# Optimization experiments

Hardware: AMD Instinct MI355X
Metric: run time of the kernel (lower is better)

The kernel has to match this reference:

```python
import jax, jax.numpy as jnp
import numpy as np

B, T, E, H, M = 1, 2048, 1536, 16, 3
KVH = 8
NREP = H // KVH
HD = E // H // M  # 32
EPS = 1e-5


def setup_inputs() -> dict:
    key = jax.random.key(0)
    ks = jax.random.split(key, 6)
    x = jax.random.normal(ks[0], (B, T, E), jnp.float32)
    # true rotary tables: freqs = pos * 10000^{-2i/d}, shape [T, HD//2]
    inv_freq = 1.0 / (10000.0 ** (np.arange(0, HD, 2, dtype=np.float64) / HD))
    ang = np.outer(np.arange(T, dtype=np.float64), inv_freq)
    cos = jnp.asarray(np.cos(ang), jnp.float32)
    sin = jnp.asarray(np.sin(ang), jnp.float32)
    s = 0.02
    q_w = s * jax.random.normal(ks[1], (M, E // M, E), jnp.float32)
    k_w = s * jax.random.normal(ks[2], (M, E // M // NREP, E), jnp.float32)
    v_w = s * jax.random.normal(ks[3], (E // NREP, E), jnp.float32)
    out_w = s * jax.random.normal(ks[4], (E, E), jnp.float32)
    raw_map_weights = jnp.array([0.1, -0.1, 0.1], jnp.float32)
    weight_scale = jnp.ones((1,), jnp.float32)
    subln_w = jnp.ones((M * HD,), jnp.float32)
    return dict(x=x, cos=cos, sin=sin, q_w=q_w, k_w=k_w, v_w=v_w,
                out_w=out_w, raw_map_weights=raw_map_weights,
                weight_scale=weight_scale, subln_w=subln_w)


def _rope_interleaved(t, cos, sin):
    # t: [..., seq, heads, hd]; cos/sin: [seq, hd//2]
    x1 = t[..., 0::2]
    x2 = t[..., 1::2]
    c = cos[:, None, :]
    s = sin[:, None, :]
    o1 = x1 * c - x2 * s
    o2 = x1 * s + x2 * c
    return jnp.stack([o1, o2], axis=-1).reshape(t.shape)


def reference(x, cos, sin, q_w, k_w, v_w, out_w, raw_map_weights, weight_scale, subln_w):
    b, t, e = x.shape
    m = q_w.shape[0]
    hd = 2 * cos.shape[-1]
    h = q_w.shape[1] // hd
    kvh = k_w.shape[1] // hd
    nrep = h // kvh
    scaling = hd ** -0.5

    map_w = jnp.tanh(raw_map_weights) * weight_scale  # [M]

    # per-map Q/K projections, all maps at once
    q = jnp.einsum('bte,mfe->mbtf', x, q_w).reshape(m, b, t, h, hd)
    k = jnp.einsum('bte,mfe->mbtf', x, k_w).reshape(m, b, t, kvh, hd)
    q = _rope_interleaved(q, cos, sin) * scaling
    k = _rope_interleaved(k, cos, sin)
    q = q.transpose(0, 1, 3, 2, 4)                      # [m,b,h,t,hd]
    k = jnp.repeat(k.transpose(0, 1, 3, 2, 4), nrep, axis=2)  # [m,b,h,t,hd]

    v = jnp.einsum('bte,fe->btf', x, v_w).reshape(b, t, kvh, m * hd)
    v = jnp.repeat(v.transpose(0, 2, 1, 3), nrep, axis=1)  # [b,h,t,m*hd]

    causal = jnp.where(jnp.triu(jnp.ones((t, t), bool), 1),
                       jnp.float32(-jnp.inf), jnp.float32(0.0))

    scores = jnp.einsum('mbhtd,mbhsd->mbhts', q, k)
    scores = jnp.nan_to_num(scores) + causal
    attn_w = jax.nn.softmax(scores.astype(jnp.float32), axis=-1).astype(x.dtype)
    combined = jnp.einsum('m,mbhts->bhts', map_w, attn_w)

    attn = jnp.einsum('bhts,bhsf->bhtf', combined, v)  # [b,h,t,m*hd]
    # RMSNorm over last dim
    var = jnp.mean(jnp.square(attn.astype(jnp.float32)), axis=-1, keepdims=True)
    attn = (attn * jax.lax.rsqrt(var + EPS)).astype(attn.dtype) * subln_w

    attn = attn.transpose(0, 2, 1, 3).reshape(b, t, h * m * hd)
    return jnp.einsum('bte,fe->btf', attn, out_w)
```

## Files before the change

kernel.cpp:

```cpp
#include <hip/hip_runtime.h>
#include <hip/hip_bf16.h>
#include <math.h>

#define T_DIM 2048
#define E_DIM 1536
#define K_DIM 1536

typedef unsigned short u16;
typedef unsigned int u32;
typedef __attribute__((ext_vector_type(8))) short bf16x8;
typedef __attribute__((ext_vector_type(4))) float f32x4;

__device__ __forceinline__ u16 f2bf(float x) {
    unsigned u = __float_as_uint(x);
    return (u16)((u + 0x7fffu + ((u >> 16) & 1u)) >> 16);
}

#define GLOAD16(gsrc, ldst)                                                              \
    __builtin_amdgcn_global_load_lds((const __attribute__((address_space(1))) u32*)(gsrc), \
                                     (__attribute__((address_space(3))) u32*)(ldst), 16, 0, 0)

__global__ __launch_bounds__(256) void cvt_bf16_5(const float* __restrict__ s0, u16* __restrict__ d0,
                                                  const float* __restrict__ s1, u16* __restrict__ d1,
                                                  const float* __restrict__ s2, u16* __restrict__ d2,
                                                  const float* __restrict__ s3, u16* __restrict__ d3,
                                                  const float* __restrict__ s4, u16* __restrict__ d4) {
    int i = blockIdx.x * 256 + threadIdx.x;
    const float* s;
    u16* d;
    int off;
    if (i < 786432)       { s = s0; d = d0; off = i; }
    else if (i < 1376256) { s = s1; d = d1; off = i - 786432; }
    else if (i < 1671168) { s = s2; d = d2; off = i - 1376256; }
    else if (i < 1966080) { s = s3; d = d3; off = i - 1671168; }
    else                  { s = s4; d = d4; off = i - 1966080; }
    float4 v = ((const float4*)s)[off];
    ((ushort4*)d)[off] = make_ushort4(f2bf(v.x), f2bf(v.y), f2bf(v.z), f2bf(v.w));
}

__global__ __launch_bounds__(256) void gemm_qkv_fused(const u16* __restrict__ A,
                                                      const u16* __restrict__ W,
                                                      const float* __restrict__ cosb,
                                                      const float* __restrict__ sinb,
                                                      u16* __restrict__ qb16,
                                                      u16* __restrict__ kpack,
                                                      u16* __restrict__ vpack,
                                                      float qscale) {
    const int K = K_DIM;
    __shared__ __align__(16) u16 As[128 * 64];
    __shared__ __align__(16) u16 Bs[128 * 64];
    const int tid = threadIdx.x;
    const int lane = tid & 63;
    const int wv = tid >> 6;
    const int wr = wv >> 1;
    const int wc = wv & 1;
    const int cl = lane & 15;
    const int g = lane >> 4;
    const int bm = blockIdx.y * 128;
    const int bn = blockIdx.x * 128;

    const char* Ab = (const char*)A;
    const char* Wb = (const char*)W;

    size_t a_src[4], b_src[4];
    int dst[4];
#pragma unroll
    for (int is = 0; is < 4; ++is) {
        int b = is * 4096 + tid * 16;
        int row = b >> 7;
        int wi = b & 127;
        dst[is] = b;
        a_src[is] = (size_t)(bm + row) * (K * 2) + (wi ^ ((row & 7) << 4));
        b_src[is] = (size_t)(bn + row) * (K * 2) + (wi ^ ((row & 7) << 4));
    }

    f32x4 acc[4][4];
#pragma unroll
    for (int mi = 0; mi < 4; ++mi)
#pragma unroll
        for (int ni = 0; ni < 4; ++ni) acc[mi][ni] = (f32x4){0.f, 0.f, 0.f, 0.f};

    for (int k0b = 0; k0b < K * 2; k0b += 128) {
#pragma unroll
        for (int is = 0; is < 4; ++is)
            GLOAD16(Ab + a_src[is] + k0b, (char*)As + dst[is]);
#pragma unroll
        for (int is = 0; is < 4; ++is)
            GLOAD16(Wb + b_src[is] + k0b, (char*)Bs + dst[is]);
        __syncthreads();
#pragma unroll
        for (int kk = 0; kk < 2; ++kk) {
            const int co = (kk * 64 + g * 16) ^ ((cl & 7) << 4);
            bf16x8 af[4], bfr[4];
#pragma unroll
            for (int mi = 0; mi < 4; ++mi)
                af[mi] = *(const bf16x8*)((const char*)As + (wr * 64 + mi * 16 + cl) * 128 + co);
#pragma unroll
            for (int ni = 0; ni < 4; ++ni)
                bfr[ni] = *(const bf16x8*)((const char*)Bs + (wc * 64 + ni * 16 + cl) * 128 + co);
#pragma unroll
            for (int mi = 0; mi < 4; ++mi)
#pragma unroll
                for (int ni = 0; ni < 4; ++ni)
                    acc[mi][ni] = __builtin_amdgcn_mfma_f32_16x16x32_bf16(af[mi], bfr[ni], acc[mi][ni], 0, 0, 0);
        }
        __syncthreads();
    }

    if (bn < 1536) {
#pragma unroll
        for (int mi = 0; mi < 4; ++mi)
#pragma unroll
            for (int ni = 0; ni < 4; ++ni)
#pragma unroll
                for (int r = 0; r < 4; ++r) {
                    int trow = bm + wr * 64 + mi * 16 + 4 * g + r;
                    int c = bn + wc * 64 + ni * 16 + cl;
                    float v = acc[mi][ni][r];
                    float pv = __shfl_xor(v, 1, 64);
                    int i = (c & 31) >> 1;
                    float cs = cosb[trow * 16 + i];
                    float sn = sinb[trow * 16 + i];
                    float o = v * cs + ((c & 1) ? pv * sn : -pv * sn);
                    qb16[(size_t)trow * E_DIM + c] = f2bf(o * qscale);
                }
    } else if (bn < 2304) {
#pragma unroll
        for (int mi = 0; mi < 4; ++mi)
#pragma unroll
            for (int ni = 0; ni < 4; ++ni)
#pragma unroll
                for (int r = 0; r < 4; ++r) {
                    int trow = bm + wr * 64 + mi * 16 + 4 * g + r;
                    int c = bn + wc * 64 + ni * 16 + cl;
                    float v = acc[mi][ni][r];
                    float pv = __shfl_xor(v, 1, 64);
                    int i = (c & 31) >> 1;
                    float cs = cosb[trow * 16 + i];
                    float sn = sinb[trow * 16 + i];
                    float o = v * cs + ((c & 1) ? pv * sn : -pv * sn);
                    int ck = c - 1536;
                    int m = ck >> 8;
                    int rem = ck & 255;
                    int kvhh = rem >> 5;
                    int d = rem & 31;
                    int cch = trow >> 5, st2 = (trow >> 4) & 1, colk = trow & 15;
                    size_t dstb = ((((size_t)(kvhh * 64 + cch) * 3 + m) * 2 + st2) * 16 + colk) * 32 + d;
                    kpack[dstb] = f2bf(o);
                }
    } else {
#pragma unroll
        for (int mi = 0; mi < 4; ++mi)
#pragma unroll
            for (int ni = 0; ni < 4; ++ni)
#pragma unroll
                for (int r = 0; r < 4; ++r) {
                    int trow = bm + wr * 64 + mi * 16 + 4 * g + r;
                    int c = bn + wc * 64 + ni * 16 + cl;
                    int fq = c - 2304;
                    int kvhh = fq / 96;
                    int f = fq - kvhh * 96;
                    size_t dstb = ((size_t)(kvhh * 64 + (trow >> 5)) * 96 + f) * 32 + (trow & 31);
                    vpack[dstb] = f2bf(acc[mi][ni][r]);
                }
    }
}

__global__ __launch_bounds__(256) void gemm_mfma_out(const u16* __restrict__ A,
                                                     const u16* __restrict__ W,
                                                     float* __restrict__ Cp,
                                                     int K, int ldC) {
    __shared__ __align__(16) u16 As[128 * 64];
    __shared__ __align__(16) u16 Bs[64 * 64];
    const int tid = threadIdx.x;
    const int lane = tid & 63;
    const int wv = tid >> 6;
    const int wr = wv >> 1;
    const int wc = wv & 1;
    const int cl = lane & 15;
    const int g = lane >> 4;
    const int bm = blockIdx.y * 128;
    const int bn = blockIdx.x * 64;

    const char* Ab = (const char*)A;
    const char* Wb = (const char*)W;

    size_t a_src[4];
    int a_dst[4];
#pragma unroll
    for (int is = 0; is < 4; ++is) {
        int b = is * 4096 + wv * 1024 + lane * 16;
        int row = b >> 7;
        int wi = b & 127;
        a_src[is] = (size_t)(bm + row) * (K * 2) + (wi ^ ((row & 7) << 4));
        a_dst[is] = b;
    }
    size_t b_src[2];
    int b_dst[2];
#pragma unroll
    for (int is = 0; is < 2; ++is) {
        int b = is * 4096 + wv * 1024 + lane * 16;
        int row = b >> 7;
        int wi = b & 127;
        b_src[is] = (size_t)(bn + row) * (K * 2) + (wi ^ ((row & 7) << 4));
        b_dst[is] = b;
    }

    f32x4 acc[4][2];
#pragma unroll
    for (int mi = 0; mi < 4; ++mi)
#pragma unroll
        for (int ni = 0; ni < 2; ++ni) acc[mi][ni] = (f32x4){0.f, 0.f, 0.f, 0.f};

    for (int k0b = 0; k0b < K * 2; k0b += 128) {
#pragma unroll
        for (int is = 0; is < 4; ++is)
            GLOAD16(Ab + a_src[is] + k0b, (char*)As + a_dst[is]);
#pragma unroll
        for (int is = 0; is < 2; ++is)
            GLOAD16(Wb + b_src[is] + k0b, (char*)Bs + b_dst[is]);
        __syncthreads();
#pragma unroll
        for (int kk = 0; kk < 2; ++kk) {
            const int co = (kk * 64 + g * 16) ^ ((cl & 7) << 4);
            bf16x8 af[4], bfr[2];
#pragma unroll
            for (int mi = 0; mi < 4; ++mi)
                af[mi] = *(const bf16x8*)((const char*)As + (wr * 64 + mi * 16 + cl) * 128 + co);
#pragma unroll
            for (int ni = 0; ni < 2; ++ni)
                bfr[ni] = *(const bf16x8*)((const char*)Bs + (wc * 32 + ni * 16 + cl) * 128 + co);
#pragma unroll
            for (int mi = 0; mi < 4; ++mi)
#pragma unroll
                for (int ni = 0; ni < 2; ++ni)
                    acc[mi][ni] = __builtin_amdgcn_mfma_f32_16x16x32_bf16(af[mi], bfr[ni], acc[mi][ni], 0, 0, 0);
        }
        __syncthreads();
    }

#pragma unroll
    for (int mi = 0; mi < 4; ++mi)
#pragma unroll
        for (int ni = 0; ni < 2; ++ni)
#pragma unroll
            for (int r = 0; r < 4; ++r) {
                size_t row = bm + wr * 64 + mi * 16 + 4 * g + r;
                size_t col = bn + wc * 32 + ni * 16 + cl;
                Cp[row * ldC + col] = acc[mi][ni][r];
            }
}

__device__ __forceinline__ void attn_block_map(int lid, int& h, int& qbase) {
    int kvh8 = lid & 7;
    int rest = lid >> 3;
    h = kvh8 * 2 + (rest & 1);
    qbase = (63 - (rest >> 1)) * 32;
}

__global__ __launch_bounds__(256) void attn_lsum(const u16* __restrict__ qb,
                                                 const u16* __restrict__ kpack,
                                                 const float* __restrict__ raw_map,
                                                 const float* __restrict__ wscale,
                                                 float* __restrict__ facbuf) {
    __shared__ float red1[4][3][2][16];
    const int tid = threadIdx.x;
    const int lane = tid & 63;
    const int wv = tid >> 6;
    const int col = lane & 15;
    const int g = lane >> 4;
    int h, qbase;
    attn_block_map(blockIdx.y * 64 + blockIdx.x, h, qbase);
    const int kvh = h >> 1;
    const int nfull = qbase >> 5;

    bf16x8 qfrag[3][2];
#pragma unroll
    for (int m = 0; m < 3; ++m)
#pragma unroll
        for (int q2 = 0; q2 < 2; ++q2)
            qfrag[m][q2] = *(const bf16x8*)(qb + (size_t)(qbase + 16 * q2 + col) * E_DIM + m * 512 + h * 32 + 8 * g);

    float lsum[3][2] = {{0.f, 0.f}, {0.f, 0.f}, {0.f, 0.f}};
    const int laneoff = col * 32 + 8 * g;
    const u16* kt = kpack + (size_t)(kvh * 64 + wv) * 3072;

    for (int c = wv; c < nfull; c += 4) {
        bf16x8 kf[6];
#pragma unroll
        for (int u = 0; u < 6; ++u) kf[u] = *(const bf16x8*)(kt + laneoff + u * 512);
        kt += 4 * 3072;
        __builtin_amdgcn_s_setprio(1);
#pragma unroll
        for (int m = 0; m < 3; ++m)
#pragma unroll
            for (int st = 0; st < 2; ++st)
#pragma unroll
                for (int q2 = 0; q2 < 2; ++q2) {
                    f32x4 sv = __builtin_amdgcn_mfma_f32_16x16x32_bf16(
                        kf[m * 2 + st], qfrag[m][q2], (f32x4){0.f, 0.f, 0.f, 0.f}, 0, 0, 0);
                    lsum[m][q2] += (__builtin_amdgcn_exp2f(sv[0]) + __builtin_amdgcn_exp2f(sv[1])) +
                                   (__builtin_amdgcn_exp2f(sv[2]) + __builtin_amdgcn_exp2f(sv[3]));
                }
        __builtin_amdgcn_s_setprio(0);
    }

    if ((nfull & 3) == wv) {
        const u16* ktm = kpack + (size_t)(kvh * 64 + nfull) * 3072 + laneoff;
        bf16x8 kf[6];
#pragma unroll
        for (int u = 0; u < 6; ++u) kf[u] = *(const bf16x8*)(ktm + u * 512);
#pragma unroll
        for (int m = 0; m < 3; ++m) {
            {
                f32x4 sv = __builtin_amdgcn_mfma_f32_16x16x32_bf16(
                    kf[m * 2 + 0], qfrag[m][0], (f32x4){0.f, 0.f, 0.f, 0.f}, 0, 0, 0);
#pragma unroll
                for (int r = 0; r < 4; ++r) {
                    float x = (4 * g + r > col) ? -1e30f : sv[r];
                    lsum[m][0] += __builtin_amdgcn_exp2f(x);
                }
            }
            {
                f32x4 sv = __builtin_amdgcn_mfma_f32_16x16x32_bf16(
                    kf[m * 2 + 0], qfrag[m][1], (f32x4){0.f, 0.f, 0.f, 0.f}, 0, 0, 0);
                lsum[m][1] += (__builtin_amdgcn_exp2f(sv[0]) + __builtin_amdgcn_exp2f(sv[1])) +
                              (__builtin_amdgcn_exp2f(sv[2]) + __builtin_amdgcn_exp2f(sv[3]));
            }
            {
                f32x4 sv = __builtin_amdgcn_mfma_f32_16x16x32_bf16(
                    kf[m * 2 + 1], qfrag[m][1], (f32x4){0.f, 0.f, 0.f, 0.f}, 0, 0, 0);
#pragma unroll
                for (int r = 0; r < 4; ++r) {
                    float x = (4 * g + r > col) ? -1e30f : sv[r];
                    lsum[m][1] += __builtin_amdgcn_exp2f(x);
                }
            }
        }
    }

#pragma unroll
    for (int m = 0; m < 3; ++m)
#pragma unroll
        for (int q2 = 0; q2 < 2; ++q2) {
            lsum[m][q2] += __shfl_xor(lsum[m][q2], 16, 64);
            lsum[m][q2] += __shfl_xor(lsum[m][q2], 32, 64);
        }
    if (g == 0) {
#pragma unroll
        for (int m = 0; m < 3; ++m)
#pragma unroll
            for (int q2 = 0; q2 < 2; ++q2) red1[wv][m][q2][col] = lsum[m][q2];
    }
    __syncthreads();
    if (wv == 0 && lane < 16) {
        float wsc = wscale[0];
#pragma unroll
        for (int m = 0; m < 3; ++m) {
            float mw = tanhf(raw_map[m]) * wsc;
#pragma unroll
            for (int q2 = 0; q2 < 2; ++q2) {
                float tot = red1[0][m][q2][lane] + red1[1][m][q2][lane] +
                            red1[2][m][q2][lane] + red1[3][m][q2][lane];
                facbuf[(size_t)(m * 16 + h) * T_DIM + qbase + 16 * q2 + lane] = mw / tot;
            }
        }
    }
}

__global__ __launch_bounds__(256) void attn_pv(const u16* __restrict__ qb,
                                               const u16* __restrict__ kpack,
                                               const u16* __restrict__ vpack,
                                               const float* __restrict__ facbuf,
                                               const float* __restrict__ subln,
                                               u16* __restrict__ outb) {
    __shared__ __align__(16) char smem[12288];
    const int tid = threadIdx.x;
    const int lane = tid & 63;
    const int wv = tid >> 6;
    const int col = lane & 15;
    const int g = lane >> 4;
    int h, qbase;
    attn_block_map(blockIdx.y * 64 + blockIdx.x, h, qbase);
    const int kvh = h >> 1;
    const int nfull = qbase >> 5;

    u16 (*plds)[2][16][40] = (u16(*)[2][16][40])smem;
    float (*red2)[48] = (float(*)[48])smem;

    bf16x8 qfrag[3][2];
#pragma unroll
    for (int m = 0; m < 3; ++m)
#pragma unroll
        for (int q2 = 0; q2 < 2; ++q2)
            qfrag[m][q2] = *(const bf16x8*)(qb + (size_t)(qbase + 16 * q2 + col) * E_DIM + m * 512 + h * 32 + 8 * g);

    float fac[3][2];
#pragma unroll
    for (int m = 0; m < 3; ++m)
#pragma unroll
        for (int q2 = 0; q2 < 2; ++q2)
            fac[m][q2] = facbuf[(size_t)(m * 16 + h) * T_DIM + qbase + 16 * q2 + col];

    f32x4 oacc[2][6];
#pragma unroll
    for (int q2 = 0; q2 < 2; ++q2)
#pragma unroll
        for (int ft = 0; ft < 6; ++ft) oacc[q2][ft] = (f32x4){0.f, 0.f, 0.f, 0.f};

    const int laneoff = col * 32 + 8 * g;
    const u16* kt = kpack + (size_t)(kvh * 64 + wv) * 3072;
    const u16* vt = vpack + (size_t)(kvh * 64 + wv) * 3072;

    for (int c = wv; c < nfull; c += 4) {
        bf16x8 kf[6], vf[6];
#pragma unroll
        for (int u = 0; u < 6; ++u) kf[u] = *(const bf16x8*)(kt + laneoff + u * 512);
#pragma unroll
        for (int u = 0; u < 6; ++u) vf[u] = *(const bf16x8*)(vt + laneoff + u * 512);
        kt += 4 * 3072;
        vt += 4 * 3072;

        __builtin_amdgcn_s_setprio(1);
#pragma unroll
        for (int q2 = 0; q2 < 2; ++q2)
#pragma unroll
            for (int st = 0; st < 2; ++st) {
                float p[4] = {0.f, 0.f, 0.f, 0.f};
#pragma unroll
                for (int m = 0; m < 3; ++m) {
                    f32x4 sv = __builtin_amdgcn_mfma_f32_16x16x32_bf16(
                        kf[m * 2 + st], qfrag[m][q2], (f32x4){0.f, 0.f, 0.f, 0.f}, 0, 0, 0);
#pragma unroll
                    for (int r = 0; r < 4; ++r)
                        p[r] += fac[m][q2] * __builtin_amdgcn_exp2f(sv[r]);
                }
                __hip_bfloat162 b01 = __float22bfloat162_rn(make_float2(p[0], p[1]));
                __hip_bfloat162 b23 = __float22bfloat162_rn(make_float2(p[2], p[3]));
                uint2 w;
                w.x = *(u32*)&b01;
                w.y = *(u32*)&b23;
                *(uint2*)&plds[wv][q2][col][st * 16 + 4 * g] = w;
            }
#pragma unroll
        for (int q2 = 0; q2 < 2; ++q2) {
            bf16x8 pf = *(const bf16x8*)&plds[wv][q2][col][8 * g];
#pragma unroll
            for (int ft = 0; ft < 6; ++ft)
                oacc[q2][ft] = __builtin_amdgcn_mfma_f32_16x16x32_bf16(pf, vf[ft], oacc[q2][ft], 0, 0, 0);
        }
        __builtin_amdgcn_s_setprio(0);
    }

    if ((nfull & 3) == wv) {
        const u16* ktm = kpack + (size_t)(kvh * 64 + nfull) * 3072 + laneoff;
        const u16* vtm = vpack + (size_t)(kvh * 64 + nfull) * 3072 + laneoff;
        bf16x8 kf[6], vf[6];
#pragma unroll
        for (int u = 0; u < 6; ++u) kf[u] = *(const bf16x8*)(ktm + u * 512);
#pragma unroll
        for (int u = 0; u < 6; ++u) vf[u] = *(const bf16x8*)(vtm + u * 512);

        {
            float p[4] = {0.f, 0.f, 0.f, 0.f};
#pragma unroll
            for (int m = 0; m < 3; ++m) {
                f32x4 sv = __builtin_amdgcn_mfma_f32_16x16x32_bf16(
                    kf[m * 2 + 0], qfrag[m][0], (f32x4){0.f, 0.f, 0.f, 0.f}, 0, 0, 0);
#pragma unroll
                for (int r = 0; r < 4; ++r) {
                    float x = (4 * g + r > col) ? -1e30f : sv[r];
                    p[r] += fac[m][0] * __builtin_amdgcn_exp2f(x);
                }
            }
            __hip_bfloat162 b01 = __float22bfloat162_rn(make_float2(p[0], p[1]));
            __hip_bfloat162 b23 = __float22bfloat162_rn(make_float2(p[2], p[3]));
            uint2 w;
            w.x = *(u32*)&b01;
            w.y = *(u32*)&b23;
            *(uint2*)&plds[wv][0][col][4 * g] = w;
            uint2 z = make_uint2(0u, 0u);
            *(uint2*)&plds[wv][0][col][16 + 4 * g] = z;
        }
        {
            float p0[4] = {0.f, 0.f, 0.f, 0.f};
            float p1[4] = {0.f, 0.f, 0.f, 0.f};
#pragma unroll
            for (int m = 0; m < 3; ++m) {
                f32x4 sv0 = __builtin_amdgcn_mfma_f32_16x16x32_bf16(
                    kf[m * 2 + 0], qfrag[m][1], (f32x4){0.f, 0.f, 0.f, 0.f}, 0, 0, 0);
                f32x4 sv1 = __builtin_amdgcn_mfma_f32_16x16x32_bf16(
                    kf[m * 2 + 1], qfrag[m][1], (f32x4){0.f, 0.f, 0.f, 0.f}, 0, 0, 0);
#pragma unroll
                for (int r = 0; r < 4; ++r) {
                    p0[r] += fac[m][1] * __builtin_amdgcn_exp2f(sv0[r]);
                    float x = (4 * g + r > col) ? -1e30f : sv1[r];
                    p1[r] += fac[m][1] * __builtin_amdgcn_exp2f(x);
                }
            }
            __hip_bfloat162 a01 = __float22bfloat162_rn(make_float2(p0[0], p0[1]));
            __hip_bfloat162 a23 = __float22bfloat162_rn(make_float2(p0[2], p0[3]));
            uint2 w0;
            w0.x = *(u32*)&a01;
            w0.y = *(u32*)&a23;
            *(uint2*)&plds[wv][1][col][4 * g] = w0;
            __hip_bfloat162 b01 = __float22bfloat162_rn(make_float2(p1[0], p1[1]));
            __hip_bfloat162 b23 = __float22bfloat162_rn(make_float2(p1[2], p1[3]));
            uint2 w1;
            w1.x = *(u32*)&b01;
            w1.y = *(u32*)&b23;
            *(uint2*)&plds[wv][1][col][16 + 4 * g] = w1;
        }
#pragma unroll
        for (int q2 = 0; q2 < 2; ++q2) {
            bf16x8 pf = *(const bf16x8*)&plds[wv][q2][col][8 * g];
#pragma unroll
            for (int ft = 0; ft < 6; ++ft)
                oacc[q2][ft] = __builtin_amdgcn_mfma_f32_16x16x32_bf16(pf, vf[ft], oacc[q2][ft], 0, 0, 0);
        }
    }

    __syncthreads();
#pragma unroll
    for (int src = 1; src < 4; ++src) {
        if (wv == src) {
            float4* rp = (float4*)red2[lane];
#pragma unroll
            for (int q2 = 0; q2 < 2; ++q2)
#pragma unroll
                for (int ft = 0; ft < 6; ++ft)
                    rp[q2 * 6 + ft] = make_float4(oacc[q2][ft][0], oacc[q2][ft][1],
                                                  oacc[q2][ft][2], oacc[q2][ft][3]);
        }
        __syncthreads();
        if (wv == 0) {
            const float4* rp = (const float4*)red2[lane];
#pragma unroll
            for (int q2 = 0; q2 < 2; ++q2)
#pragma unroll
                for (int ft = 0; ft < 6; ++ft) {
                    float4 a = rp[q2 * 6 + ft];
                    oacc[q2][ft][0] += a.x; oacc[q2][ft][1] += a.y;
                    oacc[q2][ft][2] += a.z; oacc[q2][ft][3] += a.w;
                }
        }
        __syncthreads();
    }
    if (wv != 0) return;

    float ss[2][4] = {{0.f, 0.f, 0.f, 0.f}, {0.f, 0.f, 0.f, 0.f}};
#pragma unroll
    for (int q2 = 0; q2 < 2; ++q2)
#pragma unroll
        for (int ft = 0; ft < 6; ++ft)
#pragma unroll
            for (int r = 0; r < 4; ++r) ss[q2][r] += oacc[q2][ft][r] * oacc[q2][ft][r];
#pragma unroll
    for (int q2 = 0; q2 < 2; ++q2)
#pragma unroll
        for (int r = 0; r < 4; ++r) {
            ss[q2][r] += __shfl_xor(ss[q2][r], 1, 64);
            ss[q2][r] += __shfl_xor(ss[q2][r], 2, 64);
            ss[q2][r] += __shfl_xor(ss[q2][r], 4, 64);
            ss[q2][r] += __shfl_xor(ss[q2][r], 8, 64);
            ss[q2][r] = rsqrtf(ss[q2][r] * (1.f / 96.f) + 1e-5f);
        }
#pragma unroll
    for (int ft = 0; ft < 6; ++ft) {
        float sl = subln[ft * 16 + col];
#pragma unroll
        for (int q2 = 0; q2 < 2; ++q2)
#pragma unroll
            for (int r = 0; r < 4; ++r) {
                int trow = qbase + 16 * q2 + 4 * g + r;
                outb[(size_t)trow * E_DIM + h * 96 + ft * 16 + col] = f2bf(oacc[q2][ft][r] * ss[q2][r] * sl);
            }
    }
}

extern "C" void kernel_launch(void* const* d_in, const int* in_sizes, int n_in,
                              void* d_out, int out_size, void* d_ws, size_t ws_size,
                              hipStream_t stream) {
    const float* x       = (const float*)d_in[0];
    const float* cosb    = (const float*)d_in[1];
    const float* sinb    = (const float*)d_in[2];
    const float* q_w     = (const float*)d_in[3];
    const float* k_w     = (const float*)d_in[4];
    const float* v_w     = (const float*)d_in[5];
    const float* out_w   = (const float*)d_in[6];
    const float* raw_map = (const float*)d_in[7];
    const float* wscale  = (const float*)d_in[8];
    const float* subln   = (const float*)d_in[9];
    float* out = (float*)d_out;

    char* ws = (char*)d_ws;
    u16* xb16   = (u16*)(ws);
    u16* wqkv16 = (u16*)(ws + 6291456);
    u16* qb16   = (u16*)(ws + 15728640);
    u16* kpack  = (u16*)(ws + 22020096);
    u16* vpack  = (u16*)(ws + 25190400);
    u16* wout16 = (u16*)(ws + 28360704);
    float* facbuf = (float*)(ws + 33079296);
    u16* ab16   = xb16;

    cvt_bf16_5<<<9984, 256, 0, stream>>>(x, xb16,
                                         q_w, wqkv16,
                                         k_w, wqkv16 + 2359296,
                                         v_w, wqkv16 + 3538944,
                                         out_w, wout16);

    const float qscale = 0.17677669529663687f * 1.4426950408889634f;
    gemm_qkv_fused<<<dim3(3072 / 128, T_DIM / 128), 256, 0, stream>>>(
        xb16, wqkv16, cosb, sinb, qb16, kpack, vpack, qscale);

    attn_lsum<<<dim3(64, 16), 256, 0, stream>>>(qb16, kpack, raw_map, wscale, facbuf);

    attn_pv<<<dim3(64, 16), 256, 0, stream>>>(qb16, kpack, vpack, facbuf, subln, ab16);

    gemm_mfma_out<<<dim3(E_DIM / 64, T_DIM / 128), 256, 0, stream>>>(ab16, wout16, out, K_DIM, E_DIM);
}
```

Measured before the change: 131.2 us.

## Fuse softmax-sum and PV attention kernels with paired causal query tiles

Merges the two attention kernels (row-sum pass and PV pass) into one kernel. The per-row normalization factors now stay in LDS instead of going through a global buffer, which saves a launch and the facbuf round trip. Each block handles two query tiles, one early and one late (qt=63-p and qt=p), so causal work per block is balanced and the grid shrinks from 1024 to 512 blocks. The cost is fewer blocks for latency hiding, serial dependence within each block, and the added syncs between the two halves.

```diff
diff --git a/kernel.cpp b/kernel.cpp
--- a/kernel.cpp
+++ b/kernel.cpp
@@ -251,330 +251,305 @@
             }
 }
 
-__device__ __forceinline__ void attn_block_map(int lid, int& h, int& qbase) {
-    int kvh8 = lid & 7;
-    int rest = lid >> 3;
-    h = kvh8 * 2 + (rest & 1);
-    qbase = (63 - (rest >> 1)) * 32;
-}
-
-__global__ __launch_bounds__(256) void attn_lsum(const u16* __restrict__ qb,
-                                                 const u16* __restrict__ kpack,
-                                                 const float* __restrict__ raw_map,
-                                                 const float* __restrict__ wscale,
-                                                 float* __restrict__ facbuf) {
-    __shared__ float red1[4][3][2][16];
-    const int tid = threadIdx.x;
-    const int lane = tid & 63;
-    const int wv = tid >> 6;
-    const int col = lane & 15;
-    const int g = lane >> 4;
-    int h, qbase;
-    attn_block_map(blockIdx.y * 64 + blockIdx.x, h, qbase);
-    const int kvh = h >> 1;
-    const int nfull = qbase >> 5;
-
-    bf16x8 qfrag[3][2];
-#pragma unroll
-    for (int m = 0; m < 3; ++m)
-#pragma unroll
-        for (int q2 = 0; q2 < 2; ++q2)
-            qfrag[m][q2] = *(const bf16x8*)(qb + (size_t)(qbase + 16 * q2 + col) * E_DIM + m * 512 + h * 32 + 8 * g);
-
-    float lsum[3][2] = {{0.f, 0.f}, {0.f, 0.f}, {0.f, 0.f}};
-    const int laneoff = col * 32 + 8 * g;
-    const u16* kt = kpack + (size_t)(kvh * 64 + wv) * 3072;
-
-    for (int c = wv; c < nfull; c += 4) {
-        bf16x8 kf[6];
-#pragma unroll
-        for (int u = 0; u < 6; ++u) kf[u] = *(const bf16x8*)(kt + laneoff + u * 512);
-        kt += 4 * 3072;
-        __builtin_amdgcn_s_setprio(1);
-#pragma unroll
-        for (int m = 0; m < 3; ++m)
-#pragma unroll
-            for (int st = 0; st < 2; ++st)
-#pragma unroll
-                for (int q2 = 0; q2 < 2; ++q2) {
-                    f32x4 sv = __builtin_amdgcn_mfma_f32_16x16x32_bf16(
-                        kf[m * 2 + st], qfrag[m][q2], (f32x4){0.f, 0.f, 0.f, 0.f}, 0, 0, 0);
-                    lsum[m][q2] += (__builtin_amdgcn_exp2f(sv[0]) + __builtin_amdgcn_exp2f(sv[1])) +
-                                   (__builtin_amdgcn_exp2f(sv[2]) + __builtin_amdgcn_exp2f(sv[3]));
-                }
-        __builtin_amdgcn_s_setprio(0);
-    }
-
-    if ((nfull & 3) == wv) {
-        const u16* ktm = kpack + (size_t)(kvh * 64 + nfull) * 3072 + laneoff;
-        bf16x8 kf[6];
-#pragma unroll
-        for (int u = 0; u < 6; ++u) kf[u] = *(const bf16x8*)(ktm + u * 512);
-#pragma unroll
-        for (int m = 0; m < 3; ++m) {
-            {
-                f32x4 sv = __builtin_amdgcn_mfma_f32_16x16x32_bf16(
-                    kf[m * 2 + 0], qfrag[m][0], (f32x4){0.f, 0.f, 0.f, 0.f}, 0, 0, 0);
-#pragma unroll
-                for (int r = 0; r < 4; ++r) {
-                    float x = (4 * g + r > col) ? -1e30f : sv[r];
-                    lsum[m][0] += __builtin_amdgcn_exp2f(x);
-                }
-            }
-            {
-                f32x4 sv = __builtin_amdgcn_mfma_f32_16x16x32_bf16(
-                    kf[m * 2 + 0], qfrag[m][1], (f32x4){0.f, 0.f, 0.f, 0.f}, 0, 0, 0);
-                lsum[m][1] += (__builtin_amdgcn_exp2f(sv[0]) + __builtin_amdgcn_exp2f(sv[1])) +
-                              (__builtin_amdgcn_exp2f(sv[2]) + __builtin_amdgcn_exp2f(sv[3]));
-            }
-            {
-                f32x4 sv = __builtin_amdgcn_mfma_f32_16x16x32_bf16(
-                    kf[m * 2 + 1], qfrag[m][1], (f32x4){0.f, 0.f, 0.f, 0.f}, 0, 0, 0);
-#pragma unroll
-                for (int r = 0; r < 4; ++r) {
-                    float x = (4 * g + r > col) ? -1e30f : sv[r];
-                    lsum[m][1] += __builtin_amdgcn_exp2f(x);
-                }
-            }
-        }
-    }
-
-#pragma unroll
-    for (int m = 0; m < 3; ++m)
-#pragma unroll
-        for (int q2 = 0; q2 < 2; ++q2) {
-            lsum[m][q2] += __shfl_xor(lsum[m][q2], 16, 64);
-            lsum[m][q2] += __shfl_xor(lsum[m][q2], 32, 64);
-        }
-    if (g == 0) {
-#pragma unroll
-        for (int m = 0; m < 3; ++m)
-#pragma unroll
-            for (int q2 = 0; q2 < 2; ++q2) red1[wv][m][q2][col] = lsum[m][q2];
-    }
-    __syncthreads();
-    if (wv == 0 && lane < 16) {
-        float wsc = wscale[0];
-#pragma unroll
-        for (int m = 0; m < 3; ++m) {
-            float mw = tanhf(raw_map[m]) * wsc;
-#pragma unroll
-            for (int q2 = 0; q2 < 2; ++q2) {
-                float tot = red1[0][m][q2][lane] + red1[1][m][q2][lane] +
-                            red1[2][m][q2][lane] + red1[3][m][q2][lane];
-                facbuf[(size_t)(m * 16 + h) * T_DIM + qbase + 16 * q2 + lane] = mw / tot;
-            }
-        }
-    }
-}
-
-__global__ __launch_bounds__(256) void attn_pv(const u16* __restrict__ qb,
-                                               const u16* __restrict__ kpack,
-                                               const u16* __restrict__ vpack,
-                                               const float* __restrict__ facbuf,
-                                               const float* __restrict__ subln,
-                                               u16* __restrict__ outb) {
+__global__ __launch_bounds__(256) void attn_fused(const u16* __restrict__ qb,
+                                                  const u16* __restrict__ kpack,
+                                                  const u16* __restrict__ vpack,
+                                                  const float* __restrict__ raw_map,
+                                                  const float* __restrict__ wscale,
+                                                  const float* __restrict__ subln,
+                                                  u16* __restrict__ outb) {
     __shared__ __align__(16) char smem[12288];
     const int tid = threadIdx.x;
     const int lane = tid & 63;
     const int wv = tid >> 6;
     const int col = lane & 15;
     const int g = lane >> 4;
-    int h, qbase;
-    attn_block_map(blockIdx.y * 64 + blockIdx.x, h, qbase);
-    const int kvh = h >> 1;
-    const int nfull = qbase >> 5;
+    const int lid = blockIdx.x;
+    const int kvh = lid & 7;
+    const int rest = lid >> 3;
+    const int h = kvh * 2 + (rest & 1);
+    const int p = rest >> 1;
 
     u16 (*plds)[2][16][40] = (u16(*)[2][16][40])smem;
     float (*red2)[48] = (float(*)[48])smem;
-
-    bf16x8 qfrag[3][2];
-#pragma unroll
-    for (int m = 0; m < 3; ++m)
+    float (*red1)[3][2][16] = (float(*)[3][2][16])smem;
+
+    float mw[3];
+    {
+        float wsc = wscale[0];
+#pragma unroll
+        for (int m = 0; m < 3; ++m) mw[m] = tanhf(raw_map[m]) * wsc;
+    }
+    const int laneoff = col * 32 + 8 * g;
+
+    for (int half = 0; half < 2; ++half) {
+        const int qt = half ? p : (63 - p);
+        const int qbase = qt * 32;
+        const int nfull = qt;
+
+        bf16x8 qfrag[3][2];
+#pragma unroll
+        for (int m = 0; m < 3; ++m)
+#pragma unroll
+            for (int q2 = 0; q2 < 2; ++q2)
+                qfrag[m][q2] = *(const bf16x8*)(qb + (size_t)(qbase + 16 * q2 + col) * E_DIM + m * 512 + h * 32 + 8 * g);
+
+        float lsum[3][2] = {{0.f, 0.f}, {0.f, 0.f}, {0.f, 0.f}};
+        {
+            const u16* kt = kpack + (size_t)(kvh * 64 + wv) * 3072;
+            for (int c = wv; c < nfull; c += 4) {
+                bf16x8 kf[6];
+#pragma unroll
+                for (int u = 0; u < 6; ++u) kf[u] = *(const bf16x8*)(kt + laneoff + u * 512);
+                kt += 4 * 3072;
+                __builtin_amdgcn_s_setprio(1);
+#pragma unroll
+                for (int m = 0; m < 3; ++m)
+#pragma unroll
+                    for (int st = 0; st < 2; ++st)
+#pragma unroll
+                        for (int q2 = 0; q2 < 2; ++q2) {
+                            f32x4 sv = __builtin_amdgcn_mfma_f32_16x16x32_bf16(
+                                kf[m * 2 + st], qfrag[m][q2], (f32x4){0.f, 0.f, 0.f, 0.f}, 0, 0, 0);
+                            lsum[m][q2] += (__builtin_amdgcn_exp2f(sv[0]) + __builtin_amdgcn_exp2f(sv[1])) +
+                                           (__builtin_amdgcn_exp2f(sv[2]) + __builtin_amdgcn_exp2f(sv[3]));
+                        }
+                __builtin_amdgcn_s_setprio(0);
+            }
+            if ((nfull & 3) == wv) {
+                const u16* ktm = kpack + (size_t)(kvh * 64 + nfull) * 3072 + laneoff;
+                bf16x8 kf[6];
+#pragma unroll
+                for (int u = 0; u < 6; ++u) kf[u] = *(const bf16x8*)(ktm + u * 512);
+#pragma unroll
+                for (int m = 0; m < 3; ++m) {
+                    {
+                        f32x4 sv = __builtin_amdgcn_mfma_f32_16x16x32_bf16(
+                            kf[m * 2 + 0], qfrag[m][0], (f32x4){0.f, 0.f, 0.f, 0.f}, 0, 0, 0);
+#pragma unroll
+                        for (int r = 0; r < 4; ++r) {
+                            float x = (4 * g + r > col) ? -1e30f : sv[r];
+                            lsum[m][0] += __builtin_amdgcn_exp2f(x);
+                        }
+                    }
+                    {
+                        f32x4 sv = __builtin_amdgcn_mfma_f32_16x16x32_bf16(
+                            kf[m * 2 + 0], qfrag[m][1], (f32x4){0.f, 0.f, 0.f, 0.f}, 0, 0, 0);
+                        lsum[m][1] += (__builtin_amdgcn_exp2f(sv[0]) + __builtin_amdgcn_exp2f(sv[1])) +
+                                      (__builtin_amdgcn_exp2f(sv[2]) + __builtin_amdgcn_exp2f(sv[3]));
+                    }
+                    {
+                        f32x4 sv = __builtin_amdgcn_mfma_f32_16x16x32_bf16(
+                            kf[m * 2 + 1], qfrag[m][1], (f32x4){0.f, 0.f, 0.f, 0.f}, 0, 0, 0);
+#pragma unroll
+                        for (int r = 0; r < 4; ++r) {
+                            float x = (4 * g + r > col) ? -1e30f : sv[r];
+                            lsum[m][1] += __builtin_amdgcn_exp2f(x);
+                        }
+                    }
+                }
+            }
+        }
+#pragma unroll
+        for (int m = 0; m < 3; ++m)
+#pragma unroll
+            for (int q2 = 0; q2 < 2; ++q2) {
+                lsum[m][q2] += __shfl_xor(lsum[m][q2], 16, 64);
+                lsum[m][q2] += __shfl_xor(lsum[m][q2], 32, 64);
+            }
+        if (g == 0) {
+#pragma unroll
+            for (int m = 0; m < 3; ++m)
+#pragma unroll
+                for (int q2 = 0; q2 < 2; ++q2) red1[wv][m][q2][col] = lsum[m][q2];
+        }
+        __syncthreads();
+        float fac[3][2];
+#pragma unroll
+        for (int m = 0; m < 3; ++m)
+#pragma unroll
+            for (int q2 = 0; q2 < 2; ++q2)
+                fac[m][q2] = mw[m] / (red1[0][m][q2][col] + red1[1][m][q2][col] +
+                                      red1[2][m][q2][col] + red1[3][m][q2][col]);
+        __syncthreads();
+
+        f32x4 oacc[2][6];
 #pragma unroll
         for (int q2 = 0; q2 < 2; ++q2)
-            qfrag[m][q2] = *(const bf16x8*)(qb + (size_t)(qbase + 16 * q2 + col) * E_DIM + m * 512 + h * 32 + 8 * g);
-
-    float fac[3][2];
-#pragma unroll
-    for (int m = 0; m < 3; ++m)
-#pragma unroll
-        for (int q2 = 0; q2 < 2; ++q2)
-            fac[m][q2] = facbuf[(size_t)(m * 16 + h) * T_DIM + qbase + 16 * q2 + col];
-
-    f32x4 oacc[2][6];
-#pragma unroll
-    for (int q2 = 0; q2 < 2; ++q2)
-#pragma unroll
-        for (int ft = 0; ft < 6; ++ft) oacc[q2][ft] = (f32x4){0.f, 0.f, 0.f, 0.f};
-
-    const int laneoff = col * 32 + 8 * g;
-    const u16* kt = kpack + (size_t)(kvh * 64 + wv) * 3072;
-    const u16* vt = vpack + (size_t)(kvh * 64 + wv) * 3072;
-
-    for (int c = wv; c < nfull; c += 4) {
-        bf16x8 kf[6], vf[6];
-#pragma unroll
-        for (int u = 0; u < 6; ++u) kf[u] = *(const bf16x8*)(kt + laneoff + u * 512);
-#pragma unroll
-        for (int u = 0; u < 6; ++u) vf[u] = *(const bf16x8*)(vt + laneoff + u * 512);
-        kt += 4 * 3072;
-        vt += 4 * 3072;
-
-        __builtin_amdgcn_s_setprio(1);
-#pragma unroll
-        for (int q2 = 0; q2 < 2; ++q2)
-#pragma unroll
-            for (int st = 0; st < 2; ++st) {
-                float p[4] = {0.f, 0.f, 0.f, 0.f};
-#pragma unroll
-                for (int m = 0; m < 3; ++m) {
-                    f32x4 sv = __builtin_amdgcn_mfma_f32_16x16x32_bf16(
-                        kf[m * 2 + st], qfrag[m][q2], (f32x4){0.f, 0.f, 0.f, 0.f}, 0, 0, 0);
-#pragma unroll
-                    for (int r = 0; r < 4; ++r)
-                        p[r] += fac[m][q2] * __builtin_amdgcn_exp2f(sv[r]);
-                }
-                __hip_bfloat162 b01 = __float22bfloat162_rn(make_float2(p[0], p[1]));
-                __hip_bfloat162 b23 = __float22bfloat162_rn(make_float2(p[2], p[3]));
-                uint2 w;
-                w.x = *(u32*)&b01;
-                w.y = *(u32*)&b23;
-                *(uint2*)&plds[wv][q2][col][st * 16 + 4 * g] = w;
-            }
-#pragma unroll
-        for (int q2 = 0; q2 < 2; ++q2) {
-            bf16x8 pf = *(const bf16x8*)&plds[wv][q2][col][8 * g];
-#pragma unroll
-            for (int ft = 0; ft < 6; ++ft)
-                oacc[q2][ft] = __builtin_amdgcn_mfma_f32_16x16x32_bf16(pf, vf[ft], oacc[q2][ft], 0, 0, 0);
-        }
-        __builtin_amdgcn_s_setprio(0);
-    }
-
-    if ((nfull & 3) == wv) {
-        const u16* ktm = kpack + (size_t)(kvh * 64 + nfull) * 3072 + laneoff;
-        const u16* vtm = vpack + (size_t)(kvh * 64 + nfull) * 3072 + laneoff;
-        bf16x8 kf[6], vf[6];
-#pragma unroll
-        for (int u = 0; u < 6; ++u) kf[u] = *(const bf16x8*)(ktm + u * 512);
-#pragma unroll
-        for (int u = 0; u < 6; ++u) vf[u] = *(const bf16x8*)(vtm + u * 512);
+#pragma unroll
+            for (int ft = 0; ft < 6; ++ft) oacc[q2][ft] = (f32x4){0.f, 0.f, 0.f, 0.f};
 
         {
-            float p[4] = {0.f, 0.f, 0.f, 0.f};
-#pragma unroll
-            for (int m = 0; m < 3; ++m) {
-                f32x4 sv = __builtin_amdgcn_mfma_f32_16x16x32_bf16(
-                    kf[m * 2 + 0], qfrag[m][0], (f32x4){0.f, 0.f, 0.f, 0.f}, 0, 0, 0);
+            const u16* kt = kpack + (size_t)(kvh * 64 + wv) * 3072;
+            const u16* vt = vpack + (size_t)(kvh * 64 + wv) * 3072;
+            for (int c = wv; c < nfull; c += 4) {
+                bf16x8 kf[6], vf[6];
+#pragma unroll
+                for (int u = 0; u < 6; ++u) kf[u] = *(const bf16x8*)(kt + laneoff + u * 512);
+#pragma unroll
+                for (int u = 0; u < 6; ++u) vf[u] = *(const bf16x8*)(vt + laneoff + u * 512);
+                kt += 4 * 3072;
+                vt += 4 * 3072;
+
+                __builtin_amdgcn_s_setprio(1);
+#pragma unroll
+                for (int q2 = 0; q2 < 2; ++q2)
+#pragma unroll
+                    for (int st = 0; st < 2; ++st) {
+                        float pp[4] = {0.f, 0.f, 0.f, 0.f};
+#pragma unroll
+                        for (int m = 0; m < 3; ++m) {
+                            f32x4 sv = __builtin_amdgcn_mfma_f32_16x16x32_bf16(
+                                kf[m * 2 + st], qfrag[m][q2], (f32x4){0.f, 0.f, 0.f, 0.f}, 0, 0, 0);
+#pragma unroll
+                            for (int r = 0; r < 4; ++r)
+                                pp[r] += fac[m][q2] * __builtin_amdgcn_exp2f(sv[r]);
+                        }
+                        __hip_bfloat162 b01 = __float22bfloat162_rn(make_float2(pp[0], pp[1]));
+                        __hip_bfloat162 b23 = __float22bfloat162_rn(make_float2(pp[2], pp[3]));
+                        uint2 w;
+                        w.x = *(u32*)&b01;
+                        w.y = *(u32*)&b23;
+                        *(uint2*)&plds[wv][q2][col][st * 16 + 4 * g] = w;
+                    }
+#pragma unroll
+                for (int q2 = 0; q2 < 2; ++q2) {
+                    bf16x8 pf = *(const bf16x8*)&plds[wv][q2][col][8 * g];
+#pragma unroll
+                    for (int ft = 0; ft < 6; ++ft)
+                        oacc[q2][ft] = __builtin_amdgcn_mfma_f32_16x16x32_bf16(pf, vf[ft], oacc[q2][ft], 0, 0, 0);
+                }
+                __builtin_amdgcn_s_setprio(0);
+            }
+
+            if ((nfull & 3) == wv) {
+                const u16* ktm = kpack + (size_t)(kvh * 64 + nfull) * 3072 + laneoff;
+                const u16* vtm = vpack + (size_t)(kvh * 64 + nfull) * 3072 + laneoff;
+                bf16x8 kf[6], vf[6];
+#pragma unroll
+                for (int u = 0; u < 6; ++u) kf[u] = *(const bf16x8*)(ktm + u * 512);
+#pragma unroll
+                for (int u = 0; u < 6; ++u) vf[u] = *(const bf16x8*)(vtm + u * 512);
+
+                {
+                    float pp[4] = {0.f, 0.f, 0.f, 0.f};
+#pragma unroll
+                    for (int m = 0; m < 3; ++m) {
+                        f32x4 sv = __builtin_amdgcn_mfma_f32_16x16x32_bf16(
+                            kf[m * 2 + 0], qfrag[m][0], (f32x4){0.f, 0.f, 0.f, 0.f}, 0, 0, 0);
+#pragma unroll
+                        for (int r = 0; r < 4; ++r) {
+                            float x = (4 * g + r > col) ? -1e30f : sv[r];
+                            pp[r] += fac[m][0] * __builtin_amdgcn_exp2f(x);
+                        }
+                    }
+                    __hip_bfloat162 b01 = __float22bfloat162_rn(make_float2(pp[0], pp[1]));
+                    __hip_bfloat162 b23 = __float22bfloat162_rn(make_float2(pp[2], pp[3]));
+                    uint2 w;
+                    w.x = *(u32*)&b01;
+                    w.y = *(u32*)&b23;
+                    *(uint2*)&plds[wv][0][col][4 * g] = w;
+                    uint2 z = make_uint2(0u, 0u);
+                    *(uint2*)&plds[wv][0][col][16 + 4 * g] = z;
+                }
+                {
+                    float p0[4] = {0.f, 0.f, 0.f, 0.f};
+                    float p1[4] = {0.f, 0.f, 0.f, 0.f};
+#pragma unroll
+                    for (int m = 0; m < 3; ++m) {
+                        f32x4 sv0 = __builtin_amdgcn_mfma_f32_16x16x32_bf16(
+                            kf[m * 2 + 0], qfrag[m][1], (f32x4){0.f, 0.f, 0.f, 0.f}, 0, 0, 0);
+                        f32x4 sv1 = __builtin_amdgcn_mfma_f32_16x16x32_bf16(
+                            kf[m * 2 + 1], qfrag[m][1], (f32x4){0.f, 0.f, 0.f, 0.f}, 0, 0, 0);
+#pragma unroll
+                        for (int r = 0; r < 4; ++r) {
+                            p0[r] += fac[m][1] * __builtin_amdgcn_exp2f(sv0[r]);
+                            float x = (4 * g + r > col) ? -1e30f : sv1[r];
+                            p1[r] += fac[m][1] * __builtin_amdgcn_exp2f(x);
+                        }
+                    }
+                    __hip_bfloat162 a01 = __float22bfloat162_rn(make_float2(p0[0], p0[1]));
+                    __hip_bfloat162 a23 = __float22bfloat162_rn(make_float2(p0[2], p0[3]));
+                    uint2 w0;
+                    w0.x = *(u32*)&a01;
+                    w0.y = *(u32*)&a23;
+                    *(uint2*)&plds[wv][1][col][4 * g] = w0;
+                    __hip_bfloat162 b01 = __float22bfloat162_rn(make_float2(p1[0], p1[1]));
+                    __hip_bfloat162 b23 = __float22bfloat162_rn(make_float2(p1[2], p1[3]));
+                    uint2 w1;
+                    w1.x = *(u32*)&b01;
+                    w1.y = *(u32*)&b23;
+                    *(uint2*)&plds[wv][1][col][16 + 4 * g] = w1;
+                }
+#pragma unroll
+                for (int q2 = 0; q2 < 2; ++q2) {
+                    bf16x8 pf = *(const bf16x8*)&plds[wv][q2][col][8 * g];
+#pragma unroll
+                    for (int ft = 0; ft < 6; ++ft)
+                        oacc[q2][ft] = __builtin_amdgcn_mfma_f32_16x16x32_bf16(pf, vf[ft], oacc[q2][ft], 0, 0, 0);
+                }
+            }
+        }
+
+        __syncthreads();
+#pragma unroll
+        for (int src = 1; src < 4; ++src) {
+            if (wv == src) {
+                float4* rp = (float4*)red2[lane];
+#pragma unroll
+                for (int q2 = 0; q2 < 2; ++q2)
+#pragma unroll
+                    for (int ft = 0; ft < 6; ++ft)
+                        rp[q2 * 6 + ft] = make_float4(oacc[q2][ft][0], oacc[q2][ft][1],
+                                                      oacc[q2][ft][2], oacc[q2][ft][3]);
+            }
+            __syncthreads();
+            if (wv == 0) {
+                const float4* rp = (const float4*)red2[lane];
+#pragma unroll
+                for (int q2 = 0; q2 < 2; ++q2)
+#pragma unroll
+                    for (int ft = 0; ft < 6; ++ft) {
+                        float4 a = rp[q2 * 6 + ft];
+                        oacc[q2][ft][0] += a.x; oacc[q2][ft][1] += a.y;
+                        oacc[q2][ft][2] += a.z; oacc[q2][ft][3] += a.w;
+                    }
+            }
+            __syncthreads();
+        }
+
+        if (wv == 0) {
+            float ss[2][4] = {{0.f, 0.f, 0.f, 0.f}, {0.f, 0.f, 0.f, 0.f}};
+#pragma unroll
+            for (int q2 = 0; q2 < 2; ++q2)
+#pragma unroll
+                for (int ft = 0; ft < 6; ++ft)
+#pragma unroll
+                    for (int r = 0; r < 4; ++r) ss[q2][r] += oacc[q2][ft][r] * oacc[q2][ft][r];
+#pragma unroll
+            for (int q2 = 0; q2 < 2; ++q2)
 #pragma unroll
                 for (int r = 0; r < 4; ++r) {
-                    float x = (4 * g + r > col) ? -1e30f : sv[r];
-                    p[r] += fac[m][0] * __builtin_amdgcn_exp2f(x);
-                }
-            }
-            __hip_bfloat162 b01 = __float22bfloat162_rn(make_float2(p[0], p[1]));
-            __hip_bfloat162 b23 = __float22bfloat162_rn(make_float2(p[2], p[3]));
-            uint2 w;
-            w.x = *(u32*)&b01;
-            w.y = *(u32*)&b23;
-            *(uint2*)&plds[wv][0][col][4 * g] = w;
-            uint2 z = make_uint2(0u, 0u);
-            *(uint2*)&plds[wv][0][col][16 + 4 * g] = z;
-        }
-        {
-            float p0[4] = {0.f, 0.f, 0.f, 0.f};
-            float p1[4] = {0.f, 0.f, 0.f, 0.f};
-#pragma unroll
-            for (int m = 0; m < 3; ++m) {
-                f32x4 sv0 = __builtin_amdgcn_mfma_f32_16x16x32_bf16(
-                    kf[m * 2 + 0], qfrag[m][1], (f32x4){0.f, 0.f, 0.f, 0.f}, 0, 0, 0);
-                f32x4 sv1 = __builtin_amdgcn_mfma_f32_16x16x32_bf16(
-                    kf[m * 2 + 1], qfrag[m][1], (f32x4){0.f, 0.f, 0.f, 0.f}, 0, 0, 0);
-#pragma unroll
-                for (int r = 0; r < 4; ++r) {
-                    p0[r] += fac[m][1] * __builtin_amdgcn_exp2f(sv0[r]);
-                    float x = (4 * g + r > col) ? -1e30f : sv1[r];
-                    p1[r] += fac[m][1] * __builtin_amdgcn_exp2f(x);
-                }
-            }
-            __hip_bfloat162 a01 = __float22bfloat162_rn(make_float2(p0[0], p0[1]));
-            __hip_bfloat162 a23 = __float22bfloat162_rn(make_float2(p0[2], p0[3]));
-            uint2 w0;
-            w0.x = *(u32*)&a01;
-            w0.y = *(u32*)&a23;
-            *(uint2*)&plds[wv][1][col][4 * g] = w0;
-            __hip_bfloat162 b01 = __float22bfloat162_rn(make_float2(p1[0], p1[1]));
-            __hip_bfloat162 b23 = __float22bfloat162_rn(make_float2(p1[2], p1[3]));
-            uint2 w1;
-            w1.x = *(u32*)&b01;
-            w1.y = *(u32*)&b23;
-            *(uint2*)&plds[wv][1][col][16 + 4 * g] = w1;
-        }
-#pragma unroll
-        for (int q2 = 0; q2 < 2; ++q2) {
-            bf16x8 pf = *(const bf16x8*)&plds[wv][q2][col][8 * g];
-#pragma unroll
-            for (int ft = 0; ft < 6; ++ft)
-                oacc[q2][ft] = __builtin_amdgcn_mfma_f32_16x16x32_bf16(pf, vf[ft], oacc[q2][ft], 0, 0, 0);
-        }
-    }
-
-    __syncthreads();
-#pragma unroll
-    for (int src = 1; src < 4; ++src) {
-        if (wv == src) {
-            float4* rp = (float4*)red2[lane];
-#pragma unroll
-            for (int q2 = 0; q2 < 2; ++q2)
-#pragma unroll
-                for (int ft = 0; ft < 6; ++ft)
-                    rp[q2 * 6 + ft] = make_float4(oacc[q2][ft][0], oacc[q2][ft][1],
-                                                  oacc[q2][ft][2], oacc[q2][ft][3]);
-        }
-        __syncthreads();
-        if (wv == 0) {
-            const float4* rp = (const float4*)red2[lane];
-#pragma unroll
-            for (int q2 = 0; q2 < 2; ++q2)
-#pragma unroll
-                for (int ft = 0; ft < 6; ++ft) {
-                    float4 a = rp[q2 * 6 + ft];
-                    oacc[q2][ft][0] += a.x; oacc[q2][ft][1] += a.y;
-                    oacc[q2][ft][2] += a.z; oacc[q2][ft][3] += a.w;
-                }
-        }
-        __syncthreads();
-    }
-    if (wv != 0) return;
-
-    float ss[2][4] = {{0.f, 0.f, 0.f, 0.f}, {0.f, 0.f, 0.f, 0.f}};
-#pragma unroll
-    for (int q2 = 0; q2 < 2; ++q2)
-#pragma unroll
-        for (int ft = 0; ft < 6; ++ft)
-#pragma unroll
-            for (int r = 0; r < 4; ++r) ss[q2][r] += oacc[q2][ft][r] * oacc[q2][ft][r];
-#pragma unroll
-    for (int q2 = 0; q2 < 2; ++q2)
-#pragma unroll
-        for (int r = 0; r < 4; ++r) {
-            ss[q2][r] += __shfl_xor(ss[q2][r], 1, 64);
-            ss[q2][r] += __shfl_xor(ss[q2][r], 2, 64);
-            ss[q2][r] += __shfl_xor(ss[q2][r], 4, 64);
-            ss[q2][r] += __shfl_xor(ss[q2][r], 8, 64);
-            ss[q2][r] = rsqrtf(ss[q2][r] * (1.f / 96.f) + 1e-5f);
-        }
-#pragma unroll
-    for (int ft = 0; ft < 6; ++ft) {
-        float sl = subln[ft * 16 + col];
-#pragma unroll
-        for (int q2 = 0; q2 < 2; ++q2)
-#pragma unroll
-            for (int r = 0; r < 4; ++r) {
-                int trow = qbase + 16 * q2 + 4 * g + r;
-                outb[(size_t)trow * E_DIM + h * 96 + ft * 16 + col] = f2bf(oacc[q2][ft][r] * ss[q2][r] * sl);
-            }
+                    ss[q2][r] += __shfl_xor(ss[q2][r], 1, 64);
+                    ss[q2][r] += __shfl_xor(ss[q2][r], 2, 64);
+                    ss[q2][r] += __shfl_xor(ss[q2][r], 4, 64);
+                    ss[q2][r] += __shfl_xor(ss[q2][r], 8, 64);
+                    ss[q2][r] = rsqrtf(ss[q2][r] * (1.f / 96.f) + 1e-5f);
+                }
+#pragma unroll
+            for (int ft = 0; ft < 6; ++ft) {
+                float sl = subln[ft * 16 + col];
+#pragma unroll
+                for (int q2 = 0; q2 < 2; ++q2)
+#pragma unroll
+                    for (int r = 0; r < 4; ++r) {
+                        int trow = qbase + 16 * q2 + 4 * g + r;
+                        outb[(size_t)trow * E_DIM + h * 96 + ft * 16 + col] =
+                            f2bf(oacc[q2][ft][r] * ss[q2][r] * sl);
+                    }
+            }
+        }
+        __syncthreads();
     }
 }
 
@@ -600,7 +575,6 @@
     u16* kpack  = (u16*)(ws + 22020096);
     u16* vpack  = (u16*)(ws + 25190400);
     u16* wout16 = (u16*)(ws + 28360704);
-    float* facbuf = (float*)(ws + 33079296);
     u16* ab16   = xb16;
 
     cvt_bf16_5<<<9984, 256, 0, stream>>>(x, xb16,
@@ -613,9 +587,7 @@
     gemm_qkv_fused<<<dim3(3072 / 128, T_DIM / 128), 256, 0, stream>>>(
         xb16, wqkv16, cosb, sinb, qb16, kpack, vpack, qscale);
 
-    attn_lsum<<<dim3(64, 16), 256, 0, stream>>>(qb16, kpack, raw_map, wscale, facbuf);
-
-    attn_pv<<<dim3(64, 16), 256, 0, stream>>>(qb16, kpack, vpack, facbuf, subln, ab16);
+    attn_fused<<<512, 256, 0, stream>>>(qb16, kpack, vpack, raw_map, wscale, subln, ab16);
 
     gemm_mfma_out<<<dim3(E_DIM / 64, T_DIM / 128), 256, 0, stream>>>(ab16, wout16, out, K_DIM, E_DIM);
 }
```

Result: faster. 127.4 us (-2.9%).
